# Performance work log

Measured on AMD Instinct MI355X. Metric: run time of the kernel, lower is better.

## Reference

```python
import jax, jax.numpy as jnp
import numpy as np

B, N, C, H = 2, 2048, 512, 8
D = C // H
SCALE = D ** (-0.5)


def setup_inputs() -> dict:
    key = jax.random.key(0)
    k1, k2, k3 = jax.random.split(key, 3)
    x = jax.random.normal(k1, (B, N, C), dtype=jnp.float32)
    qkv_w = jax.random.normal(k2, (C, 3 * C), dtype=jnp.float32) * (C ** -0.5)
    proj_w = jax.random.normal(k3, (C, C), dtype=jnp.float32) * (C ** -0.5)
    proj_b = jnp.zeros((C,), dtype=jnp.float32)
    return {"x": x, "qkv_w": qkv_w, "proj_w": proj_w, "proj_b": proj_b}


def reference(x, qkv_w, proj_w, proj_b):
    # qkv projection (no bias) -> (B, N, 3, H, D) -> (3, B, H, N, D)
    qkv = jnp.einsum('bnc,cf->bnf', x, qkv_w)
    qkv = qkv.reshape(B, N, 3, H, D).transpose(2, 0, 3, 1, 4)
    q, k, v = qkv[0], qkv[1], qkv[2]
    q = q * SCALE
    attn = jnp.einsum('bhid,bhjd->bhij', q, k)          # (B, H, N, N)
    attn = jax.nn.softmax(attn, axis=-1)
    out = jnp.einsum('bhij,bhjd->bhid', attn, v)         # (B, H, N, D)
    # Faithful to source: reshape (B,H,N,D) -> (B,N,C) WITHOUT transposing
    out = out.reshape(B, N, C)
    out = jnp.einsum('bnc,cd->bnd', out, proj_w) + proj_b
    return out
```

## Files before the change

kernel.cpp:

```cpp
#include <hip/hip_runtime.h>
#include <math.h>

constexpr int Bb = 2;
constexpr int Nn = 2048;
constexpr int Cc = 512;
constexpr int Hh = 8;
constexpr int Dd = 64;

typedef short short8 __attribute__((ext_vector_type(8)));
typedef float floatx4 __attribute__((ext_vector_type(4)));
typedef float floatx16 __attribute__((ext_vector_type(16)));

__device__ inline short8 bcs8(uint4 u) { return __builtin_bit_cast(short8, u); }

__device__ inline floatx4 mfma16(short8 a, short8 b, floatx4 c) {
    return __builtin_amdgcn_mfma_f32_16x16x32_bf16(a, b, c, 0, 0, 0);
}
__device__ inline floatx16 mfma32(short8 a, short8 b, floatx16 c) {
    return __builtin_amdgcn_mfma_f32_32x32x16_bf16(a, b, c, 0, 0, 0);
}

typedef __attribute__((address_space(1))) void gvoid;
typedef __attribute__((address_space(3))) void svoid;
__device__ inline void glds16(const void* g, void* l) {
    __builtin_amdgcn_global_load_lds((const gvoid*)g, (svoid*)l, 16, 0, 0);
}

__device__ inline unsigned pk_trunc(float a, float b) {
    return __builtin_amdgcn_perm(__float_as_uint(b), __float_as_uint(a), 0x07060302u);
}
__device__ inline unsigned pk_rne(float a, float b) {
    unsigned ua = __float_as_uint(a); ua += 0x7fffu + ((ua >> 16) & 1u);
    unsigned ub = __float_as_uint(b); ub += 0x7fffu + ((ub >> 16) & 1u);
    return __builtin_amdgcn_perm(ub, ua, 0x07060302u);
}
__device__ inline unsigned short rne1(float a) {
    unsigned u = __float_as_uint(a); u += 0x7fffu + ((u >> 16) & 1u);
    return (unsigned short)(u >> 16);
}
__device__ inline float tr16(float a) {
    return __uint_as_float(__float_as_uint(a) & 0xffff0000u);
}
__device__ inline void split8(float4 A, float4 B, uint4& hi, uint4& lo) {
    hi = make_uint4(pk_trunc(A.x, A.y), pk_trunc(A.z, A.w),
                    pk_trunc(B.x, B.y), pk_trunc(B.z, B.w));
    lo = make_uint4(pk_trunc(A.x - tr16(A.x), A.y - tr16(A.y)),
                    pk_trunc(A.z - tr16(A.z), A.w - tr16(A.w)),
                    pk_trunc(B.x - tr16(B.x), B.y - tr16(B.y)),
                    pk_trunc(B.z - tr16(B.z), B.w - tr16(B.w)));
}

__global__ __launch_bounds__(256) void wprep(const float* __restrict__ qkv_w,
                                             const float* __restrict__ proj_w,
                                             unsigned short* __restrict__ wqh,
                                             unsigned short* __restrict__ wql,
                                             unsigned short* __restrict__ wph,
                                             unsigned short* __restrict__ wpl)
{
    __shared__ float Tl[64][68];
    int bid = blockIdx.x;
    const float* src; unsigned short *dh, *dlo; int W, f0, k0;
    if (bid < 192) { int kt = bid / 24, ft = bid % 24; W = 1536; src = qkv_w; dh = wqh; dlo = wql; f0 = ft * 64; k0 = kt * 64; }
    else { int b2 = bid - 192; int kt = b2 / 8, ft = b2 % 8; W = 512; src = proj_w; dh = wph; dlo = wpl; f0 = ft * 64; k0 = kt * 64; }
    int t = threadIdx.x;
    {
        int kl = t >> 2, fc = (t & 3) * 16;
        const float* p = src + (size_t)(k0 + kl) * W + f0 + fc;
        #pragma unroll
        for (int i = 0; i < 4; ++i) {
            float4 v = *(const float4*)(p + i * 4);
            Tl[kl][fc + i * 4 + 0] = v.x; Tl[kl][fc + i * 4 + 1] = v.y;
            Tl[kl][fc + i * 4 + 2] = v.z; Tl[kl][fc + i * 4 + 3] = v.w;
        }
    }
    __syncthreads();
    {
        int fl = t >> 2, kc = (t & 3) * 16;
        float v[16];
        #pragma unroll
        for (int i = 0; i < 16; ++i) v[i] = Tl[kc + i][fl];
        unsigned hi[8], lo[8];
        #pragma unroll
        for (int i = 0; i < 8; ++i) {
            float a = v[2 * i], b = v[2 * i + 1];
            hi[i] = pk_trunc(a, b);
            lo[i] = pk_trunc(a - tr16(a), b - tr16(b));
        }
        unsigned short* oh = dh + (size_t)(f0 + fl) * 512 + k0 + kc;
        unsigned short* ol = dlo + (size_t)(f0 + fl) * 512 + k0 + kc;
        *(uint4*)oh = make_uint4(hi[0], hi[1], hi[2], hi[3]);
        *(uint4*)(oh + 8) = make_uint4(hi[4], hi[5], hi[6], hi[7]);
        *(uint4*)ol = make_uint4(lo[0], lo[1], lo[2], lo[3]);
        *(uint4*)(ol + 8) = make_uint4(lo[4], lo[5], lo[6], lo[7]);
    }
}

__global__ __launch_bounds__(256, 3) void gemm_qkv(const float* __restrict__ x,
                                                   const unsigned short* __restrict__ wh,
                                                   const unsigned short* __restrict__ wl,
                                                   unsigned short* __restrict__ qkvb)
{
    __shared__ __align__(16) char smem[28672];
    char* Ah = smem; char* Al = smem + 8192; char* Bh = smem + 16384; char* Bl = smem + 22528;
    const int tid = threadIdx.x, lane = tid & 63, w = tid >> 6;
    const int l15 = lane & 15, l4 = lane >> 4;
    const int row0 = blockIdx.y * 128, col0 = blockIdx.x * 96;
    const int wm = w >> 1, wn = w & 1;

    floatx4 acc[4][3];
    #pragma unroll
    for (int i = 0; i < 4; ++i)
        #pragma unroll
        for (int j = 0; j < 3; ++j)
            #pragma unroll
            for (int r = 0; r < 4; ++r) acc[i][j][r] = 0.f;

    for (int k0 = 0; k0 < 512; k0 += 32) {
        #pragma unroll
        for (int i = 0; i < 3; ++i) {
            int sid = w * 3 + i; int comp = sid & 1, nt = sid >> 1;
            const unsigned short* src = (comp ? wl : wh) + (size_t)(col0 + nt * 16 + l15) * 512 + k0 + l4 * 8;
            glds16(src, (comp ? Bl : Bh) + nt * 1024);
        }
        {
            int m = tid >> 1, q2 = (tid & 1) * 2;
            const float* px = x + (size_t)(row0 + m) * 512 + k0 + q2 * 8;
            float4 a = *(const float4*)px, b = *(const float4*)(px + 4);
            float4 c = *(const float4*)(px + 8), d = *(const float4*)(px + 12);
            uint4 h0, L0, h1, L1;
            split8(a, b, h0, L0); split8(c, d, h1, L1);
            int seg = (m >> 4) * 1024;
            int off0 = seg + (((q2) << 4) | (m & 15)) * 16;
            int off1 = seg + (((q2 + 1) << 4) | (m & 15)) * 16;
            *(uint4*)(Ah + off0) = h0; *(uint4*)(Al + off0) = L0;
            *(uint4*)(Ah + off1) = h1; *(uint4*)(Al + off1) = L1;
        }
        __syncthreads();
        short8 af[4][2], bf[3][2];
        #pragma unroll
        for (int mt = 0; mt < 4; ++mt) {
            int off = ((wm * 4 + mt) << 10) + (lane << 4);
            af[mt][0] = bcs8(*(const uint4*)(Ah + off));
            af[mt][1] = bcs8(*(const uint4*)(Al + off));
        }
        #pragma unroll
        for (int nt = 0; nt < 3; ++nt) {
            int off = ((wn * 3 + nt) << 10) + (lane << 4);
            bf[nt][0] = bcs8(*(const uint4*)(Bh + off));
            bf[nt][1] = bcs8(*(const uint4*)(Bl + off));
        }
        #pragma unroll
        for (int mt = 0; mt < 4; ++mt)
            #pragma unroll
            for (int nt = 0; nt < 3; ++nt) {
                acc[mt][nt] = mfma16(af[mt][0], bf[nt][0], acc[mt][nt]);
                acc[mt][nt] = mfma16(af[mt][0], bf[nt][1], acc[mt][nt]);
                acc[mt][nt] = mfma16(af[mt][1], bf[nt][0], acc[mt][nt]);
            }
        __syncthreads();
    }
    #pragma unroll
    for (int mt = 0; mt < 4; ++mt)
        #pragma unroll
        for (int nt = 0; nt < 3; ++nt) {
            int c = col0 + (wn * 3 + nt) * 16 + l15;
            float s = (c < 512) ? 0.125f : 1.0f;
            #pragma unroll
            for (int r = 0; r < 4; ++r) {
                int tok = row0 + (wm * 4 + mt) * 16 + l4 * 4 + r;
                qkvb[(size_t)tok * 1536 + c] = rne1(acc[mt][nt][r] * s);
            }
        }
}

__global__ __launch_bounds__(256) void vtrans(const unsigned short* __restrict__ qkvb,
                                              unsigned short* __restrict__ vt)
{
    __shared__ unsigned short Tb[64][72];
    int bh = blockIdx.x >> 5, n0 = (blockIdx.x & 31) * 64;
    int b = bh >> 3, hh = bh & 7;
    int t = threadIdx.x;
    {
        int nl = t >> 2, dc = (t & 3) * 16;
        const unsigned short* src = qkvb + (size_t)(b * 2048 + n0 + nl) * 1536 + 1024 + hh * 64 + dc;
        unsigned short tmp[16];
        *(uint4*)tmp = *(const uint4*)src;
        *(uint4*)(tmp + 8) = *(const uint4*)(src + 8);
        #pragma unroll
        for (int i = 0; i < 16; ++i) Tb[dc + i][nl] = tmp[i];
    }
    __syncthreads();
    {
        int dl = t >> 2, nc = (t & 3) * 16;
        uint4 v0 = *(const uint4*)&Tb[dl][nc];
        uint4 v1 = *(const uint4*)&Tb[dl][nc + 8];
        unsigned short* dst = vt + (size_t)(bh * 64 + dl) * 2048 + n0 + nc;
        *(uint4*)dst = v0; *(uint4*)(dst + 8) = v1;
    }
}

__global__ __launch_bounds__(512, 2) void attn(const unsigned short* __restrict__ qkvb,
                                               const unsigned short* __restrict__ vt,
                                               unsigned short* __restrict__ Oh,
                                               unsigned short* __restrict__ Ol)
{
    extern __shared__ __align__(16) char smem[];
    char* Kst = smem;
    char* Vst = smem + 32768;

    int bid = blockIdx.x;
    int xcd = bid & 7, tq = bid >> 3;
    int qb = tq & 15;
    int bh = ((tq >> 4) << 3) | xcd;
    int b = bh >> 3, hh = bh & 7;
    int tid = threadIdx.x, lane = tid & 63, w = tid >> 6;
    int qg = w >> 2, kg = w & 3;
    int l31 = lane & 31, h = lane >> 5;
    int tok0 = b * 2048 + qb * 128;

    short8 qf[2][4];
    #pragma unroll
    for (int nt = 0; nt < 2; ++nt)
        #pragma unroll
        for (int s = 0; s < 4; ++s) {
            const unsigned short* qs = qkvb + (size_t)(tok0 + qg * 64 + nt * 32 + l31) * 1536 + hh * 64 + s * 16 + h * 8;
            qf[nt][s] = bcs8(*(const uint4*)qs);
        }

    floatx16 OT[2][2];
    #pragma unroll
    for (int i = 0; i < 2; ++i)
        #pragma unroll
        for (int j = 0; j < 2; ++j)
            #pragma unroll
            for (int r = 0; r < 16; ++r) OT[i][j][r] = 0.f;
    float lacc[2] = {0.f, 0.f};

    for (int ks0 = 0; ks0 < 2048; ks0 += 256) {
        #pragma unroll
        for (int i = 0; i < 4; ++i) {
            int sid = w * 4 + i; int mt = sid >> 2, s = sid & 3;
            const unsigned short* src = qkvb + (size_t)(b * 2048 + ks0 + mt * 32 + l31) * 1536 + 512 + hh * 64 + s * 16 + h * 8;
            glds16(src, Kst + ((mt << 2) + s) * 1024);
        }
        #pragma unroll
        for (int i = 0; i < 4; ++i) {
            int sid = w * 4 + i; int mtv = sid >> 4, sv = sid & 15;
            const unsigned short* src = vt + (size_t)(bh * 64 + mtv * 32 + l31) * 2048 + ks0 + sv * 16 + h * 8;
            glds16(src, Vst + ((mtv << 4) + sv) * 1024);
        }
        __syncthreads();

        #pragma unroll
        for (int u = 0; u < 2; ++u) {
            int mt = kg * 2 + u;
            short8 kf[4];
            #pragma unroll
            for (int s = 0; s < 4; ++s)
                kf[s] = bcs8(*(const uint4*)(Kst + ((mt << 2) + s) * 1024 + (lane << 4)));
            short8 vf[2][2];
            #pragma unroll
            for (int kc = 0; kc < 2; ++kc) {
                int sv = kg * 4 + u * 2 + kc;
                vf[kc][0] = bcs8(*(const uint4*)(Vst + (sv) * 1024 + (lane << 4)));
                vf[kc][1] = bcs8(*(const uint4*)(Vst + ((16 + sv)) * 1024 + (lane << 4)));
            }
            #pragma unroll
            for (int nt = 0; nt < 2; ++nt) {
                floatx16 st;
                #pragma unroll
                for (int r = 0; r < 16; ++r) st[r] = 0.f;
                #pragma unroll
                for (int s = 0; s < 4; ++s) st = mfma32(kf[s], qf[nt][s], st);
                unsigned P2[8]; float ssum = 0.f;
                #pragma unroll
                for (int s2 = 0; s2 < 8; ++s2) {
                    float e0 = __expf(st[2 * s2]), e1 = __expf(st[2 * s2 + 1]);
                    ssum += e0 + e1;
                    P2[s2] = pk_rne(e0, e1);
                }
                lacc[nt] += ssum;
                #pragma unroll
                for (int kc = 0; kc < 2; ++kc) {
                    unsigned X0 = P2[4 * kc + 0], X1 = P2[4 * kc + 1];
                    unsigned Y0 = P2[4 * kc + 2], Y1 = P2[4 * kc + 3];
                    unsigned Xo0 = __shfl_xor(X0, 32, 64), Xo1 = __shfl_xor(X1, 32, 64);
                    unsigned Yo0 = __shfl_xor(Y0, 32, 64), Yo1 = __shfl_xor(Y1, 32, 64);
                    uint4 fu;
                    fu.x = h ? Yo0 : X0;
                    fu.y = h ? Yo1 : X1;
                    fu.z = h ? Y0 : Xo0;
                    fu.w = h ? Y1 : Xo1;
                    short8 pf = bcs8(fu);
                    OT[0][nt] = mfma32(vf[kc][0], pf, OT[0][nt]);
                    OT[1][nt] = mfma32(vf[kc][1], pf, OT[1][nt]);
                }
            }
        }
        __syncthreads();
    }

    float* Mq = (float*)(smem) + qg * 4096;
    float* Lq = (float*)(smem + 32768) + qg * 128;

    if (kg == 3) {
        #pragma unroll
        for (int mtv = 0; mtv < 2; ++mtv)
            #pragma unroll
            for (int nt = 0; nt < 2; ++nt)
                #pragma unroll
                for (int r = 0; r < 16; ++r) {
                    int d = mtv * 32 + (r & 3) + 8 * (r >> 2) + 4 * h;
                    Mq[d * 64 + nt * 32 + l31] = OT[mtv][nt][r];
                }
        Lq[h * 64 + l31] = lacc[0];
        Lq[h * 64 + 32 + l31] = lacc[1];
    }
    __syncthreads();
    if (kg == 2 || kg == 1) {  }
    for (int round = 2; round >= 1; --round) {
        if (kg == round) {
            #pragma unroll
            for (int mtv = 0; mtv < 2; ++mtv)
                #pragma unroll
                for (int nt = 0; nt < 2; ++nt)
                    #pragma unroll
                    for (int r = 0; r < 16; ++r) {
                        int d = mtv * 32 + (r & 3) + 8 * (r >> 2) + 4 * h;
                        Mq[d * 64 + nt * 32 + l31] += OT[mtv][nt][r];
                    }
            Lq[h * 64 + l31] += lacc[0];
            Lq[h * 64 + 32 + l31] += lacc[1];
        }
        __syncthreads();
    }
    if (kg == 0) {
        Lq[h * 64 + l31] += lacc[0];
        Lq[h * 64 + 32 + l31] += lacc[1];
    }
    __syncthreads();
    if (kg == 0) {
        #pragma unroll
        for (int mtv = 0; mtv < 2; ++mtv)
            #pragma unroll
            for (int nt = 0; nt < 2; ++nt)
                #pragma unroll
                for (int r = 0; r < 16; ++r) {
                    int d = mtv * 32 + (r & 3) + 8 * (r >> 2) + 4 * h;
                    OT[mtv][nt][r] += Mq[d * 64 + nt * 32 + l31];
                }
        float inv0 = 1.f / (Lq[l31] + Lq[64 + l31]);
        float inv1 = 1.f / (Lq[32 + l31] + Lq[96 + l31]);
        #pragma unroll
        for (int mtv = 0; mtv < 2; ++mtv)
            #pragma unroll
            for (int r = 0; r < 16; ++r) {
                OT[mtv][0][r] *= inv0;
                OT[mtv][1][r] *= inv1;
            }
    }
    __syncthreads();
    if (kg == 0) {
        float* Tq = (float*)(smem) + qg * 4352;
        #pragma unroll
        for (int mtv = 0; mtv < 2; ++mtv)
            #pragma unroll
            for (int nt = 0; nt < 2; ++nt)
                #pragma unroll
                for (int r = 0; r < 16; ++r) {
                    int d = mtv * 32 + (r & 3) + 8 * (r >> 2) + 4 * h;
                    Tq[(nt * 32 + l31) * 68 + d] = OT[mtv][nt][r];
                }
    }
    __syncthreads();
    {
        int q = tid >> 2, dc = (tid & 3) * 16;
        const float* T = (const float*)(smem) + (q >> 6) * 4352;
        int ql = q & 63;
        float vv[16];
        #pragma unroll
        for (int i = 0; i < 16; ++i) vv[i] = T[ql * 68 + dc + i];
        unsigned hi[8], lo[8];
        #pragma unroll
        for (int i = 0; i < 8; ++i) {
            float a = vv[2 * i], bb = vv[2 * i + 1];
            hi[i] = pk_trunc(a, bb);
            lo[i] = pk_trunc(a - tr16(a), bb - tr16(bb));
        }
        size_t bo = ((size_t)(bh * 2048 + qb * 128 + q)) * 64 + dc;
        *(uint4*)(Oh + bo) = make_uint4(hi[0], hi[1], hi[2], hi[3]);
        *(uint4*)(Oh + bo + 8) = make_uint4(hi[4], hi[5], hi[6], hi[7]);
        *(uint4*)(Ol + bo) = make_uint4(lo[0], lo[1], lo[2], lo[3]);
        *(uint4*)(Ol + bo + 8) = make_uint4(lo[4], lo[5], lo[6], lo[7]);
    }
}

__global__ __launch_bounds__(512, 2) void gemm_proj(const unsigned short* __restrict__ Ah_g,
                                                    const unsigned short* __restrict__ Al_g,
                                                    const unsigned short* __restrict__ wh,
                                                    const unsigned short* __restrict__ wl,
                                                    const float* __restrict__ bias,
                                                    float* __restrict__ out)
{
    __shared__ __align__(16) char smem[24576];
    char* Ah = smem; char* Al = smem + 8192; char* Bh = smem + 16384; char* Bl = smem + 20480;
    const int tid = threadIdx.x, lane = tid & 63, w = tid >> 6;
    const int l15 = lane & 15, l4 = lane >> 4;
    const int row0 = blockIdx.y * 128, col0 = blockIdx.x * 64;
    const int wm = w >> 1, wn = w & 1;

    floatx4 acc[2][2];
    #pragma unroll
    for (int i = 0; i < 2; ++i)
        #pragma unroll
        for (int j = 0; j < 2; ++j)
            #pragma unroll
            for (int r = 0; r < 4; ++r) acc[i][j][r] = 0.f;

    for (int k0 = 0; k0 < 512; k0 += 32) {
        #pragma unroll
        for (int i = 0; i < 2; ++i) {
            int sid = w * 2 + i; int mt = sid >> 1, comp = sid & 1;
            const unsigned short* src = (comp ? Al_g : Ah_g) + (size_t)(row0 + mt * 16 + l15) * 512 + k0 + l4 * 8;
            glds16(src, (comp ? Al : Ah) + mt * 1024);
        }
        {
            int nt = w >> 1, comp = w & 1;
            const unsigned short* src = (comp ? wl : wh) + (size_t)(col0 + nt * 16 + l15) * 512 + k0 + l4 * 8;
            glds16(src, (comp ? Bl : Bh) + nt * 1024);
        }
        __syncthreads();
        short8 af[2][2], bf[2][2];
        #pragma unroll
        for (int mt = 0; mt < 2; ++mt) {
            int off = ((wm * 2 + mt) << 10) + (lane << 4);
            af[mt][0] = bcs8(*(const uint4*)(Ah + off));
            af[mt][1] = bcs8(*(const uint4*)(Al + off));
        }
        #pragma unroll
        for (int nt = 0; nt < 2; ++nt) {
            int off = ((wn * 2 + nt) << 10) + (lane << 4);
            bf[nt][0] = bcs8(*(const uint4*)(Bh + off));
            bf[nt][1] = bcs8(*(const uint4*)(Bl + off));
        }
        #pragma unroll
        for (int mt = 0; mt < 2; ++mt)
            #pragma unroll
            for (int nt = 0; nt < 2; ++nt) {
                acc[mt][nt] = mfma16(af[mt][0], bf[nt][0], acc[mt][nt]);
                acc[mt][nt] = mfma16(af[mt][0], bf[nt][1], acc[mt][nt]);
                acc[mt][nt] = mfma16(af[mt][1], bf[nt][0], acc[mt][nt]);
            }
        __syncthreads();
    }
    #pragma unroll
    for (int mt = 0; mt < 2; ++mt)
        #pragma unroll
        for (int nt = 0; nt < 2; ++nt) {
            int c = col0 + (wn * 2 + nt) * 16 + l15;
            float bv = bias[c];
            #pragma unroll
            for (int r = 0; r < 4; ++r) {
                int tok = row0 + (wm * 2 + mt) * 16 + l4 * 4 + r;
                out[(size_t)tok * 512 + c] = acc[mt][nt][r] + bv;
            }
        }
}

extern "C" void kernel_launch(void* const* d_in, const int* in_sizes, int n_in,
                              void* d_out, int out_size, void* d_ws, size_t ws_size,
                              hipStream_t stream)
{
    const float* x      = (const float*)d_in[0];
    const float* qkv_w  = (const float*)d_in[1];
    const float* proj_w = (const float*)d_in[2];
    const float* proj_b = (const float*)d_in[3];
    float* out = (float*)d_out;

    char* ws = (char*)d_ws;
    unsigned short* qkvb = (unsigned short*)ws;
    unsigned short* vt   = (unsigned short*)(ws + 12582912);
    unsigned short* wqh  = (unsigned short*)(ws + 16777216);
    unsigned short* wql  = (unsigned short*)(ws + 18350080);
    unsigned short* wph  = (unsigned short*)(ws + 19922944);
    unsigned short* wpl  = (unsigned short*)(ws + 20447232);
    unsigned short* Oh   = (unsigned short*)(ws + 20971520);
    unsigned short* Ol   = (unsigned short*)(ws + 25165824);

    wprep<<<256, 256, 0, stream>>>(qkv_w, proj_w, wqh, wql, wph, wpl);
    gemm_qkv<<<dim3(16, 32), 256, 0, stream>>>(x, wqh, wql, qkvb);
    vtrans<<<512, 256, 0, stream>>>(qkvb, vt);
    attn<<<256, 512, 65536, stream>>>(qkvb, vt, Oh, Ol);
    gemm_proj<<<dim3(8, 32), 512, 0, stream>>>(Oh, Ol, wph, wpl, proj_b, out);
}
```

Measured before the change: 165.9 us.

## Pre-split x to bf16 pairs and shrink tiles across QKV, attention and projection

Adds an xprep kernel that splits x into bf16 hi/lo arrays once, so gemm_qkv can load A tiles with direct global-to-LDS copies instead of converting inline on every K step. gemm_qkv moves to 64-column tiles (24x32 grid). Attention goes from 128-query, 512-thread blocks with dynamic LDS to 32-query, 256-thread blocks with static 32KB LDS (1024 blocks) and a simpler cross-wave reduction. gemm_proj uses 64x64 tiles with 256 threads. The goal is more blocks and higher occupancy, at the cost of an extra kernel launch, an extra pass over x in memory, and less K/V reuse per block in attention.

```diff
diff --git a/kernel.cpp b/kernel.cpp
--- a/kernel.cpp
+++ b/kernel.cpp
@@ -95,48 +95,57 @@
     }
 }
 
-__global__ __launch_bounds__(256, 3) void gemm_qkv(const float* __restrict__ x,
+__global__ __launch_bounds__(256) void xprep(const float* __restrict__ x,
+                                             unsigned short* __restrict__ xh,
+                                             unsigned short* __restrict__ xl)
+{
+    size_t base = ((size_t)blockIdx.x * 256 + threadIdx.x) * 16;
+    float4 a = *(const float4*)(x + base);
+    float4 b = *(const float4*)(x + base + 4);
+    float4 c = *(const float4*)(x + base + 8);
+    float4 d = *(const float4*)(x + base + 12);
+    uint4 h0, L0, h1, L1;
+    split8(a, b, h0, L0); split8(c, d, h1, L1);
+    *(uint4*)(xh + base) = h0; *(uint4*)(xh + base + 8) = h1;
+    *(uint4*)(xl + base) = L0; *(uint4*)(xl + base + 8) = L1;
+}
+
+__global__ __launch_bounds__(256, 3) void gemm_qkv(const unsigned short* __restrict__ xh,
+                                                   const unsigned short* __restrict__ xl,
                                                    const unsigned short* __restrict__ wh,
                                                    const unsigned short* __restrict__ wl,
                                                    unsigned short* __restrict__ qkvb)
 {
-    __shared__ __align__(16) char smem[28672];
-    char* Ah = smem; char* Al = smem + 8192; char* Bh = smem + 16384; char* Bl = smem + 22528;
+    __shared__ __align__(16) char smem[24576];
+    char* Ah = smem; char* Al = smem + 8192; char* Bh = smem + 16384; char* Bl = smem + 20480;
     const int tid = threadIdx.x, lane = tid & 63, w = tid >> 6;
     const int l15 = lane & 15, l4 = lane >> 4;
-    const int row0 = blockIdx.y * 128, col0 = blockIdx.x * 96;
+    const int row0 = blockIdx.y * 128, col0 = blockIdx.x * 64;
     const int wm = w >> 1, wn = w & 1;
 
-    floatx4 acc[4][3];
+    floatx4 acc[4][2];
     #pragma unroll
     for (int i = 0; i < 4; ++i)
         #pragma unroll
-        for (int j = 0; j < 3; ++j)
+        for (int j = 0; j < 2; ++j)
             #pragma unroll
             for (int r = 0; r < 4; ++r) acc[i][j][r] = 0.f;
 
     for (int k0 = 0; k0 < 512; k0 += 32) {
         #pragma unroll
-        for (int i = 0; i < 3; ++i) {
-            int sid = w * 3 + i; int comp = sid & 1, nt = sid >> 1;
+        for (int i = 0; i < 4; ++i) {
+            int sid = w * 4 + i; int mt = sid >> 1, comp = sid & 1;
+            const unsigned short* src = (comp ? xl : xh) + (size_t)(row0 + mt * 16 + l15) * 512 + k0 + l4 * 8;
+            glds16(src, (comp ? Al : Ah) + mt * 1024);
+        }
+        #pragma unroll
+        for (int i = 0; i < 2; ++i) {
+            int sid = w * 2 + i; int nt = sid >> 1, comp = sid & 1;
             const unsigned short* src = (comp ? wl : wh) + (size_t)(col0 + nt * 16 + l15) * 512 + k0 + l4 * 8;
             glds16(src, (comp ? Bl : Bh) + nt * 1024);
         }
-        {
-            int m = tid >> 1, q2 = (tid & 1) * 2;
-            const float* px = x + (size_t)(row0 + m) * 512 + k0 + q2 * 8;
-            float4 a = *(const float4*)px, b = *(const float4*)(px + 4);
-            float4 c = *(const float4*)(px + 8), d = *(const float4*)(px + 12);
-            uint4 h0, L0, h1, L1;
-            split8(a, b, h0, L0); split8(c, d, h1, L1);
-            int seg = (m >> 4) * 1024;
-            int off0 = seg + (((q2) << 4) | (m & 15)) * 16;
-            int off1 = seg + (((q2 + 1) << 4) | (m & 15)) * 16;
-            *(uint4*)(Ah + off0) = h0; *(uint4*)(Al + off0) = L0;
-            *(uint4*)(Ah + off1) = h1; *(uint4*)(Al + off1) = L1;
-        }
-        __syncthreads();
-        short8 af[4][2], bf[3][2];
+        __syncthreads();
+        short8 af[4][2], bf[2][2];
         #pragma unroll
         for (int mt = 0; mt < 4; ++mt) {
             int off = ((wm * 4 + mt) << 10) + (lane << 4);
@@ -144,15 +153,15 @@
             af[mt][1] = bcs8(*(const uint4*)(Al + off));
         }
         #pragma unroll
-        for (int nt = 0; nt < 3; ++nt) {
-            int off = ((wn * 3 + nt) << 10) + (lane << 4);
+        for (int nt = 0; nt < 2; ++nt) {
+            int off = ((wn * 2 + nt) << 10) + (lane << 4);
             bf[nt][0] = bcs8(*(const uint4*)(Bh + off));
             bf[nt][1] = bcs8(*(const uint4*)(Bl + off));
         }
         #pragma unroll
         for (int mt = 0; mt < 4; ++mt)
             #pragma unroll
-            for (int nt = 0; nt < 3; ++nt) {
+            for (int nt = 0; nt < 2; ++nt) {
                 acc[mt][nt] = mfma16(af[mt][0], bf[nt][0], acc[mt][nt]);
                 acc[mt][nt] = mfma16(af[mt][0], bf[nt][1], acc[mt][nt]);
                 acc[mt][nt] = mfma16(af[mt][1], bf[nt][0], acc[mt][nt]);
@@ -162,8 +171,8 @@
     #pragma unroll
     for (int mt = 0; mt < 4; ++mt)
         #pragma unroll
-        for (int nt = 0; nt < 3; ++nt) {
-            int c = col0 + (wn * 3 + nt) * 16 + l15;
+        for (int nt = 0; nt < 2; ++nt) {
+            int c = col0 + (wn * 2 + nt) * 16 + l15;
             float s = (c < 512) ? 0.125f : 1.0f;
             #pragma unroll
             for (int r = 0; r < 4; ++r) {
@@ -199,214 +208,187 @@
     }
 }
 
-__global__ __launch_bounds__(512, 2) void attn(const unsigned short* __restrict__ qkvb,
+__global__ __launch_bounds__(256, 4) void attn(const unsigned short* __restrict__ qkvb,
                                                const unsigned short* __restrict__ vt,
                                                unsigned short* __restrict__ Oh,
                                                unsigned short* __restrict__ Ol)
 {
-    extern __shared__ __align__(16) char smem[];
+    __shared__ __align__(16) char smem[32768];
     char* Kst = smem;
-    char* Vst = smem + 32768;
+    char* Vst = smem + 16384;
 
     int bid = blockIdx.x;
-    int xcd = bid & 7, tq = bid >> 3;
-    int qb = tq & 15;
-    int bh = ((tq >> 4) << 3) | xcd;
+    int xcd = bid & 7; int rr = bid >> 3;
+    int qt = rr & 63; int bhi = rr >> 6;
+    int bh = (bhi << 3) | xcd;
     int b = bh >> 3, hh = bh & 7;
-    int tid = threadIdx.x, lane = tid & 63, w = tid >> 6;
-    int qg = w >> 2, kg = w & 3;
+    int tid = threadIdx.x, lane = tid & 63, kg = tid >> 6;
     int l31 = lane & 31, h = lane >> 5;
-    int tok0 = b * 2048 + qb * 128;
-
-    short8 qf[2][4];
-    #pragma unroll
-    for (int nt = 0; nt < 2; ++nt)
-        #pragma unroll
-        for (int s = 0; s < 4; ++s) {
-            const unsigned short* qs = qkvb + (size_t)(tok0 + qg * 64 + nt * 32 + l31) * 1536 + hh * 64 + s * 16 + h * 8;
-            qf[nt][s] = bcs8(*(const uint4*)qs);
-        }
-
-    floatx16 OT[2][2];
+    int tok0 = b * 2048 + qt * 32;
+
+    short8 qf[4];
+    #pragma unroll
+    for (int s = 0; s < 4; ++s) {
+        const unsigned short* qs = qkvb + (size_t)(tok0 + l31) * 1536 + hh * 64 + s * 16 + h * 8;
+        qf[s] = bcs8(*(const uint4*)qs);
+    }
+
+    floatx16 OT[2];
     #pragma unroll
     for (int i = 0; i < 2; ++i)
         #pragma unroll
-        for (int j = 0; j < 2; ++j)
-            #pragma unroll
-            for (int r = 0; r < 16; ++r) OT[i][j][r] = 0.f;
-    float lacc[2] = {0.f, 0.f};
-
-    for (int ks0 = 0; ks0 < 2048; ks0 += 256) {
-        #pragma unroll
-        for (int i = 0; i < 4; ++i) {
-            int sid = w * 4 + i; int mt = sid >> 2, s = sid & 3;
+        for (int r = 0; r < 16; ++r) OT[i][r] = 0.f;
+    float lacc = 0.f;
+
+    for (int ks0 = 0; ks0 < 2048; ks0 += 128) {
+        #pragma unroll
+        for (int i = 0; i < 4; ++i) {
+            int sid = kg * 4 + i; int mt = sid >> 2, s = sid & 3;
             const unsigned short* src = qkvb + (size_t)(b * 2048 + ks0 + mt * 32 + l31) * 1536 + 512 + hh * 64 + s * 16 + h * 8;
             glds16(src, Kst + ((mt << 2) + s) * 1024);
         }
         #pragma unroll
         for (int i = 0; i < 4; ++i) {
-            int sid = w * 4 + i; int mtv = sid >> 4, sv = sid & 15;
+            int sid = kg * 4 + i; int mtv = sid >> 3, sv = sid & 7;
             const unsigned short* src = vt + (size_t)(bh * 64 + mtv * 32 + l31) * 2048 + ks0 + sv * 16 + h * 8;
-            glds16(src, Vst + ((mtv << 4) + sv) * 1024);
-        }
-        __syncthreads();
-
-        #pragma unroll
-        for (int u = 0; u < 2; ++u) {
-            int mt = kg * 2 + u;
-            short8 kf[4];
-            #pragma unroll
-            for (int s = 0; s < 4; ++s)
-                kf[s] = bcs8(*(const uint4*)(Kst + ((mt << 2) + s) * 1024 + (lane << 4)));
-            short8 vf[2][2];
-            #pragma unroll
-            for (int kc = 0; kc < 2; ++kc) {
-                int sv = kg * 4 + u * 2 + kc;
-                vf[kc][0] = bcs8(*(const uint4*)(Vst + (sv) * 1024 + (lane << 4)));
-                vf[kc][1] = bcs8(*(const uint4*)(Vst + ((16 + sv)) * 1024 + (lane << 4)));
-            }
-            #pragma unroll
-            for (int nt = 0; nt < 2; ++nt) {
-                floatx16 st;
-                #pragma unroll
-                for (int r = 0; r < 16; ++r) st[r] = 0.f;
-                #pragma unroll
-                for (int s = 0; s < 4; ++s) st = mfma32(kf[s], qf[nt][s], st);
-                unsigned P2[8]; float ssum = 0.f;
-                #pragma unroll
-                for (int s2 = 0; s2 < 8; ++s2) {
-                    float e0 = __expf(st[2 * s2]), e1 = __expf(st[2 * s2 + 1]);
-                    ssum += e0 + e1;
-                    P2[s2] = pk_rne(e0, e1);
-                }
-                lacc[nt] += ssum;
-                #pragma unroll
-                for (int kc = 0; kc < 2; ++kc) {
-                    unsigned X0 = P2[4 * kc + 0], X1 = P2[4 * kc + 1];
-                    unsigned Y0 = P2[4 * kc + 2], Y1 = P2[4 * kc + 3];
-                    unsigned Xo0 = __shfl_xor(X0, 32, 64), Xo1 = __shfl_xor(X1, 32, 64);
-                    unsigned Yo0 = __shfl_xor(Y0, 32, 64), Yo1 = __shfl_xor(Y1, 32, 64);
-                    uint4 fu;
-                    fu.x = h ? Yo0 : X0;
-                    fu.y = h ? Yo1 : X1;
-                    fu.z = h ? Y0 : Xo0;
-                    fu.w = h ? Y1 : Xo1;
-                    short8 pf = bcs8(fu);
-                    OT[0][nt] = mfma32(vf[kc][0], pf, OT[0][nt]);
-                    OT[1][nt] = mfma32(vf[kc][1], pf, OT[1][nt]);
-                }
-            }
-        }
-        __syncthreads();
-    }
-
-    float* Mq = (float*)(smem) + qg * 4096;
-    float* Lq = (float*)(smem + 32768) + qg * 128;
+            glds16(src, Vst + ((mtv << 3) + sv) * 1024);
+        }
+        __syncthreads();
+
+        short8 kf[4];
+        #pragma unroll
+        for (int s = 0; s < 4; ++s)
+            kf[s] = bcs8(*(const uint4*)(Kst + ((kg << 2) + s) * 1024 + (lane << 4)));
+        short8 vf[2][2];
+        #pragma unroll
+        for (int kc = 0; kc < 2; ++kc) {
+            int sv = kg * 2 + kc;
+            vf[kc][0] = bcs8(*(const uint4*)(Vst + sv * 1024 + (lane << 4)));
+            vf[kc][1] = bcs8(*(const uint4*)(Vst + (8 + sv) * 1024 + (lane << 4)));
+        }
+
+        floatx16 st;
+        #pragma unroll
+        for (int r = 0; r < 16; ++r) st[r] = 0.f;
+        #pragma unroll
+        for (int s = 0; s < 4; ++s) st = mfma32(kf[s], qf[s], st);
+
+        unsigned P2[8]; float ssum = 0.f;
+        #pragma unroll
+        for (int s2 = 0; s2 < 8; ++s2) {
+            float e0 = __expf(st[2 * s2]), e1 = __expf(st[2 * s2 + 1]);
+            ssum += e0 + e1;
+            P2[s2] = pk_rne(e0, e1);
+        }
+        lacc += ssum;
+
+        #pragma unroll
+        for (int kc = 0; kc < 2; ++kc) {
+            unsigned X0 = P2[4 * kc + 0], X1 = P2[4 * kc + 1];
+            unsigned Y0 = P2[4 * kc + 2], Y1 = P2[4 * kc + 3];
+            unsigned Xo0 = __shfl_xor(X0, 32, 64), Xo1 = __shfl_xor(X1, 32, 64);
+            unsigned Yo0 = __shfl_xor(Y0, 32, 64), Yo1 = __shfl_xor(Y1, 32, 64);
+            uint4 fu;
+            fu.x = h ? Yo0 : X0;
+            fu.y = h ? Yo1 : X1;
+            fu.z = h ? Y0 : Xo0;
+            fu.w = h ? Y1 : Xo1;
+            short8 pf = bcs8(fu);
+            OT[0] = mfma32(vf[kc][0], pf, OT[0]);
+            OT[1] = mfma32(vf[kc][1], pf, OT[1]);
+        }
+        __syncthreads();
+    }
+
+    float* Mq = (float*)smem;
+    float* Lq = (float*)(smem + 16384);
+    float* Tq = (float*)(smem + 16384 + 1024);
 
     if (kg == 3) {
         #pragma unroll
         for (int mtv = 0; mtv < 2; ++mtv)
             #pragma unroll
-            for (int nt = 0; nt < 2; ++nt)
-                #pragma unroll
-                for (int r = 0; r < 16; ++r) {
-                    int d = mtv * 32 + (r & 3) + 8 * (r >> 2) + 4 * h;
-                    Mq[d * 64 + nt * 32 + l31] = OT[mtv][nt][r];
-                }
-        Lq[h * 64 + l31] = lacc[0];
-        Lq[h * 64 + 32 + l31] = lacc[1];
-    }
-    __syncthreads();
-    if (kg == 2 || kg == 1) {  }
-    for (int round = 2; round >= 1; --round) {
-        if (kg == round) {
-            #pragma unroll
-            for (int mtv = 0; mtv < 2; ++mtv)
-                #pragma unroll
-                for (int nt = 0; nt < 2; ++nt)
-                    #pragma unroll
-                    for (int r = 0; r < 16; ++r) {
-                        int d = mtv * 32 + (r & 3) + 8 * (r >> 2) + 4 * h;
-                        Mq[d * 64 + nt * 32 + l31] += OT[mtv][nt][r];
-                    }
-            Lq[h * 64 + l31] += lacc[0];
-            Lq[h * 64 + 32 + l31] += lacc[1];
-        }
-        __syncthreads();
-    }
+            for (int r = 0; r < 16; ++r) {
+                int d = mtv * 32 + (r & 3) + 8 * (r >> 2) + 4 * h;
+                Mq[d * 32 + l31] = OT[mtv][r];
+            }
+        Lq[h * 32 + l31] = lacc;
+    }
+    __syncthreads();
+    if (kg == 2) {
+        #pragma unroll
+        for (int mtv = 0; mtv < 2; ++mtv)
+            #pragma unroll
+            for (int r = 0; r < 16; ++r) {
+                int d = mtv * 32 + (r & 3) + 8 * (r >> 2) + 4 * h;
+                Mq[d * 32 + l31] += OT[mtv][r];
+            }
+        Lq[h * 32 + l31] += lacc;
+    }
+    __syncthreads();
+    if (kg == 1) {
+        #pragma unroll
+        for (int mtv = 0; mtv < 2; ++mtv)
+            #pragma unroll
+            for (int r = 0; r < 16; ++r) {
+                int d = mtv * 32 + (r & 3) + 8 * (r >> 2) + 4 * h;
+                Mq[d * 32 + l31] += OT[mtv][r];
+            }
+        Lq[h * 32 + l31] += lacc;
+    }
+    __syncthreads();
     if (kg == 0) {
-        Lq[h * 64 + l31] += lacc[0];
-        Lq[h * 64 + 32 + l31] += lacc[1];
+        #pragma unroll
+        for (int mtv = 0; mtv < 2; ++mtv)
+            #pragma unroll
+            for (int r = 0; r < 16; ++r) {
+                int d = mtv * 32 + (r & 3) + 8 * (r >> 2) + 4 * h;
+                OT[mtv][r] += Mq[d * 32 + l31];
+            }
+        Lq[h * 32 + l31] += lacc;
     }
     __syncthreads();
     if (kg == 0) {
+        float inv = 1.f / (Lq[l31] + Lq[32 + l31]);
         #pragma unroll
         for (int mtv = 0; mtv < 2; ++mtv)
             #pragma unroll
-            for (int nt = 0; nt < 2; ++nt)
-                #pragma unroll
-                for (int r = 0; r < 16; ++r) {
-                    int d = mtv * 32 + (r & 3) + 8 * (r >> 2) + 4 * h;
-                    OT[mtv][nt][r] += Mq[d * 64 + nt * 32 + l31];
-                }
-        float inv0 = 1.f / (Lq[l31] + Lq[64 + l31]);
-        float inv1 = 1.f / (Lq[32 + l31] + Lq[96 + l31]);
-        #pragma unroll
-        for (int mtv = 0; mtv < 2; ++mtv)
-            #pragma unroll
             for (int r = 0; r < 16; ++r) {
-                OT[mtv][0][r] *= inv0;
-                OT[mtv][1][r] *= inv1;
-            }
-    }
-    __syncthreads();
-    if (kg == 0) {
-        float* Tq = (float*)(smem) + qg * 4352;
-        #pragma unroll
-        for (int mtv = 0; mtv < 2; ++mtv)
-            #pragma unroll
-            for (int nt = 0; nt < 2; ++nt)
-                #pragma unroll
-                for (int r = 0; r < 16; ++r) {
-                    int d = mtv * 32 + (r & 3) + 8 * (r >> 2) + 4 * h;
-                    Tq[(nt * 32 + l31) * 68 + d] = OT[mtv][nt][r];
-                }
+                int d = mtv * 32 + (r & 3) + 8 * (r >> 2) + 4 * h;
+                Tq[l31 * 68 + d] = OT[mtv][r] * inv;
+            }
     }
     __syncthreads();
     {
-        int q = tid >> 2, dc = (tid & 3) * 16;
-        const float* T = (const float*)(smem) + (q >> 6) * 4352;
-        int ql = q & 63;
-        float vv[16];
-        #pragma unroll
-        for (int i = 0; i < 16; ++i) vv[i] = T[ql * 68 + dc + i];
-        unsigned hi[8], lo[8];
-        #pragma unroll
-        for (int i = 0; i < 8; ++i) {
+        int q = tid >> 3, dc = (tid & 7) * 8;
+        float vv[8];
+        #pragma unroll
+        for (int i = 0; i < 8; ++i) vv[i] = Tq[q * 68 + dc + i];
+        unsigned hi[4], lo[4];
+        #pragma unroll
+        for (int i = 0; i < 4; ++i) {
             float a = vv[2 * i], bb = vv[2 * i + 1];
             hi[i] = pk_trunc(a, bb);
             lo[i] = pk_trunc(a - tr16(a), bb - tr16(bb));
         }
-        size_t bo = ((size_t)(bh * 2048 + qb * 128 + q)) * 64 + dc;
+        size_t bo = ((size_t)(bh * 2048 + qt * 32 + q)) * 64 + dc;
         *(uint4*)(Oh + bo) = make_uint4(hi[0], hi[1], hi[2], hi[3]);
-        *(uint4*)(Oh + bo + 8) = make_uint4(hi[4], hi[5], hi[6], hi[7]);
         *(uint4*)(Ol + bo) = make_uint4(lo[0], lo[1], lo[2], lo[3]);
-        *(uint4*)(Ol + bo + 8) = make_uint4(lo[4], lo[5], lo[6], lo[7]);
-    }
-}
-
-__global__ __launch_bounds__(512, 2) void gemm_proj(const unsigned short* __restrict__ Ah_g,
+    }
+}
+
+__global__ __launch_bounds__(256, 2) void gemm_proj(const unsigned short* __restrict__ Ah_g,
                                                     const unsigned short* __restrict__ Al_g,
                                                     const unsigned short* __restrict__ wh,
                                                     const unsigned short* __restrict__ wl,
                                                     const float* __restrict__ bias,
                                                     float* __restrict__ out)
 {
-    __shared__ __align__(16) char smem[24576];
-    char* Ah = smem; char* Al = smem + 8192; char* Bh = smem + 16384; char* Bl = smem + 20480;
+    __shared__ __align__(16) char smem[16384];
+    char* Ah = smem; char* Al = smem + 4096; char* Bh = smem + 8192; char* Bl = smem + 12288;
     const int tid = threadIdx.x, lane = tid & 63, w = tid >> 6;
     const int l15 = lane & 15, l4 = lane >> 4;
-    const int row0 = blockIdx.y * 128, col0 = blockIdx.x * 64;
+    const int row0 = blockIdx.y * 64, col0 = blockIdx.x * 64;
     const int wm = w >> 1, wn = w & 1;
 
     floatx4 acc[2][2];
@@ -419,15 +401,17 @@
 
     for (int k0 = 0; k0 < 512; k0 += 32) {
         #pragma unroll
-        for (int i = 0; i < 2; ++i) {
-            int sid = w * 2 + i; int mt = sid >> 1, comp = sid & 1;
-            const unsigned short* src = (comp ? Al_g : Ah_g) + (size_t)(row0 + mt * 16 + l15) * 512 + k0 + l4 * 8;
-            glds16(src, (comp ? Al : Ah) + mt * 1024);
-        }
-        {
-            int nt = w >> 1, comp = w & 1;
-            const unsigned short* src = (comp ? wl : wh) + (size_t)(col0 + nt * 16 + l15) * 512 + k0 + l4 * 8;
-            glds16(src, (comp ? Bl : Bh) + nt * 1024);
+        for (int i = 0; i < 4; ++i) {
+            int sid = w * 4 + i;
+            if (sid < 8) {
+                int mt = sid >> 1, comp = sid & 1;
+                const unsigned short* src = (comp ? Al_g : Ah_g) + (size_t)(row0 + mt * 16 + l15) * 512 + k0 + l4 * 8;
+                glds16(src, (comp ? Al : Ah) + mt * 1024);
+            } else {
+                int s2 = sid - 8; int nt = s2 >> 1, comp = s2 & 1;
+                const unsigned short* src = (comp ? wl : wh) + (size_t)(col0 + nt * 16 + l15) * 512 + k0 + l4 * 8;
+                glds16(src, (comp ? Bl : Bh) + nt * 1024);
+            }
         }
         __syncthreads();
         short8 af[2][2], bf[2][2];
@@ -486,10 +470,13 @@
     unsigned short* wpl  = (unsigned short*)(ws + 20447232);
     unsigned short* Oh   = (unsigned short*)(ws + 20971520);
     unsigned short* Ol   = (unsigned short*)(ws + 25165824);
+    unsigned short* xh = Oh;
+    unsigned short* xl = Ol;
 
     wprep<<<256, 256, 0, stream>>>(qkv_w, proj_w, wqh, wql, wph, wpl);
-    gemm_qkv<<<dim3(16, 32), 256, 0, stream>>>(x, wqh, wql, qkvb);
+    xprep<<<512, 256, 0, stream>>>(x, xh, xl);
+    gemm_qkv<<<dim3(24, 32), 256, 0, stream>>>(xh, xl, wqh, wql, qkvb);
     vtrans<<<512, 256, 0, stream>>>(qkvb, vt);
-    attn<<<256, 512, 65536, stream>>>(qkvb, vt, Oh, Ol);
-    gemm_proj<<<dim3(8, 32), 512, 0, stream>>>(Oh, Ol, wph, wpl, proj_b, out);
-}
+    attn<<<1024, 256, 0, stream>>>(qkvb, vt, Oh, Ol);
+    gemm_proj<<<dim3(8, 64), 256, 0, stream>>>(Oh, Ol, wph, wpl, proj_b, out);
+}
```

Result: slower. 204.8 us (+23.5%).
